# Performance work log

Measured on AMD Instinct MI355X. Metric: run time of the kernel, lower is better.

## Reference

```python
import jax, jax.numpy as jnp
import numpy as np

TH, TL = 0.85, 0.5          # sim thresholds
ALPHA = 0.1                 # proto EMA alpha
TEMP = 1.0                  # readout temperature
KEEP, REFINE, REPLACE, SPAWN = 0, 1, 2, 3


def _l2n(x, axis=-1):
    return x / jnp.maximum(jnp.linalg.norm(x, axis=axis, keepdims=True), 1e-12)


def setup_inputs() -> dict:
    key = jax.random.key(0)
    ks = jax.random.split(key, 12)
    B, N, C, H, W, K = 4, 8, 256, 64, 64, 16
    return {
        "value_BNCHW": jax.random.normal(ks[0], (B, N, C, H, W), jnp.float32),
        "frame_feat_BCHW": jax.random.normal(ks[1], (B, C, H, W), jnp.float32),
        "mask_BNHW": jax.random.uniform(ks[2], (B, N, H, W), jnp.float32),
        "proto": jax.random.normal(ks[3], (B, N, K, C), jnp.float32),
        "age": jax.random.uniform(ks[4], (B, N, K), jnp.float32) * 10.0,
        "usage": jax.random.uniform(ks[5], (B, N, K), jnp.float32) * 5.0,
        "conf": jax.random.uniform(ks[6], (B, N, K), jnp.float32),
        "valid": jax.random.bernoulli(ks[7], 0.7, (B, N, K)),
        "W1": jax.random.normal(ks[8], (C + K + 3 * K, 256), jnp.float32) * 0.02,
        "b1": jnp.zeros((256,), jnp.float32),
        "W2": jax.random.normal(ks[9], (256, 4), jnp.float32) * 0.02,
        "b2": jnp.zeros((4,), jnp.float32),
        "proto_gate": jnp.float32(1.0),
        "frame_gate": jnp.float32(1.0),
    }


def reference(value_BNCHW, frame_feat_BCHW, mask_BNHW, proto, age, usage, conf,
              valid, W1, b1, W2, b2, proto_gate, frame_gate):
    B, N, C, H, W = value_BNCHW.shape
    K = proto.shape[2]
    P = H * W

    # ---- candidate prototype: masked mean pool over HW ----
    flat_v = value_BNCHW.reshape(B, N, C, P)          # [B,N,C,P]
    flat_m = mask_BNHW.reshape(B, N, 1, P)            # [B,N,1,P]
    denom = flat_m.sum(-1)                            # [B,N,1]
    cand = (flat_v * flat_m).sum(-1) / jnp.maximum(denom, 1e-6)
    fallback = flat_v.mean(-1)
    cand = jnp.where(denom <= 1e-5, fallback, cand)   # [B,N,C]
    mask_strength = flat_m.mean(-1)[..., 0]           # [B,N]
    cand = _l2n(cand)

    # ---- cosine sim against bank + context ----
    norm_bank = _l2n(proto)
    sim = jnp.einsum('bnc,bnkc->bnk', cand, norm_bank)
    sim = jnp.where(valid, sim, -1.0)
    g_t = frame_feat_BCHW.mean((2, 3))                # [B,C]
    age_n = age / jnp.maximum(jax.lax.stop_gradient(age.max()), 1.0)
    use_n = usage / jnp.maximum(jax.lax.stop_gradient(usage.max()), 1.0)
    stats = jnp.stack([age_n, use_n, conf], -1).reshape(B, N, 3 * K)
    context = jnp.concatenate(
        [jnp.broadcast_to(g_t[:, None, :], (B, N, C)), sim, stats], -1)
    any_valid = valid.any(-1)
    target_slot = jnp.where(any_valid, sim.argmax(-1), 0)
    max_sim = jnp.take_along_axis(sim, target_slot[..., None], -1)[..., 0]
    max_sim = jnp.where(any_valid, max_sim, 0.0)

    # ---- policy MLP (logits logged; rule-based policy selects action) ----
    logits = jax.nn.gelu(context @ W1 + b1) @ W2 + b2  # [B,N,4]

    has_free = (~valid).any(-1)
    low = max_sim < TL
    action = jnp.full((B, N), REFINE, jnp.int32)
    action = jnp.where(max_sim > TH, KEEP, action)
    action = jnp.where(low & has_free, SPAWN, action)
    action = jnp.where(low & ~has_free, REPLACE, action)

    # ---- action-conditioned slot selection + scatter update ----
    worst = jnp.argmax(age - usage - conf + 1000.0 * (~valid), -1)
    free_slot = jnp.argmax(~valid, -1)
    spawn = action == SPAWN
    replace = action == REPLACE
    refine = action == REFINE
    keep = action == KEEP
    chosen = target_slot
    chosen = jnp.where(spawn & has_free, free_slot, chosen)
    chosen = jnp.where(spawn & ~has_free, worst, chosen)   # spawn_replace_when_full
    chosen = jnp.where(replace, worst, chosen)
    update = refine | replace | spawn
    replace_like = replace | spawn

    bi = jnp.arange(B)[:, None]
    ni = jnp.arange(N)[None, :]

    old_p = proto[bi, ni, chosen]                      # [B,N,C] gather
    refined = _l2n((1.0 - ALPHA) * old_p + ALPHA * cand)
    new_p = jnp.where(refine[..., None], refined,
                      jnp.where(replace_like[..., None], cand, old_p))
    proto_new = proto.at[bi, ni, chosen].set(new_p)

    age1 = age + 1.0
    age_new = age1.at[bi, ni, chosen].set(
        jnp.where(replace_like, 0.0, age1[bi, ni, chosen]))
    usage_new = usage.at[bi, ni, chosen].set(
        jnp.where(replace_like, 1.0,
                  usage[bi, ni, chosen] + (refine | keep).astype(jnp.float32)))
    conf_g = conf[bi, ni, chosen]
    conf_val = jnp.where(refine, jnp.clip(0.5 * conf_g + 0.5 * max_sim, 0.0, 1.0),
                         jnp.where(replace_like, jnp.clip(mask_strength, 0.0, 1.0),
                                   conf_g))
    conf_new = conf.at[bi, ni, chosen].set(conf_val)
    valid_new = valid.at[bi, ni, chosen].set(valid[bi, ni, chosen] | update)

    # ---- prototype-conditioned readout (softmax over bank slots per pixel) ----
    vn = flat_v / jnp.maximum(jnp.linalg.norm(flat_v, axis=2, keepdims=True), 1e-12)
    nb = _l2n(proto_new)
    scores = jnp.einsum('bnkc,bncp->bnkp', nb, vn) / TEMP
    scores = jnp.where(valid_new[..., None], scores, -1e9)
    wts = jax.nn.softmax(scores, axis=2)               # over K
    proto_map = jnp.einsum('bnkp,bnkc->bncp', wts, proto_new)
    proto_map = jnp.where(valid_new.any(-1)[:, :, None, None], proto_map, 0.0)
    proto_map = proto_map.reshape(B, N, C, H, W)

    conditioned = (value_BNCHW + proto_gate * proto_map
                   + frame_gate * frame_feat_BCHW[:, None])
    return conditioned, logits
```

## Files before the change

### kernel.cpp

```cpp
#include <hip/hip_runtime.h>
#include <math.h>

#define NB_B 4
#define NB_N 8
#define NB_C 256
#define NB_K 16
#define NB_P 4096
#define NB_BN (NB_B * NB_N)

typedef float nfloat4 __attribute__((ext_vector_type(4)));

#define WS_WSUM 0
#define WS_VSUM (NB_BN * NB_C)
#define WS_GT   (2 * NB_BN * NB_C)
#define WS_DEN  (WS_GT + NB_B * NB_C)
#define WS_NB   17440
#define WS_PN   (WS_NB + NB_BN * NB_K * NB_C)
#define WS_VAL  (WS_PN + NB_BN * NB_K * NB_C)

#define SLAB_STRIDE 516

__device__ __forceinline__ float2 blk_sum2(float a, float b, float2* sbuf) {
#pragma unroll
  for (int off = 32; off > 0; off >>= 1) {
    a += __shfl_down(a, off, 64);
    b += __shfl_down(b, off, 64);
  }
  int lane = threadIdx.x & 63, wid = threadIdx.x >> 6;
  __syncthreads();
  if (lane == 0) sbuf[wid] = make_float2(a, b);
  __syncthreads();
  float2 r;
  r.x = sbuf[0].x + sbuf[1].x + sbuf[2].x + sbuf[3].x;
  r.y = sbuf[0].y + sbuf[1].y + sbuf[2].y + sbuf[3].y;
  return r;
}

__device__ __forceinline__ float2 blk_max2(float a, float b, float2* sbuf) {
#pragma unroll
  for (int off = 32; off > 0; off >>= 1) {
    a = fmaxf(a, __shfl_down(a, off, 64));
    b = fmaxf(b, __shfl_down(b, off, 64));
  }
  int lane = threadIdx.x & 63, wid = threadIdx.x >> 6;
  __syncthreads();
  if (lane == 0) sbuf[wid] = make_float2(a, b);
  __syncthreads();
  float2 r;
  r.x = fmaxf(fmaxf(sbuf[0].x, sbuf[1].x), fmaxf(sbuf[2].x, sbuf[3].x));
  r.y = fmaxf(fmaxf(sbuf[0].y, sbuf[1].y), fmaxf(sbuf[2].y, sbuf[3].y));
  return r;
}

__device__ __forceinline__ int validMode(const void* vptr) {
  const unsigned int* w = (const unsigned int*)vptr;
  int mode = 0;
  for (int i = 0; i < 128; ++i) {
    unsigned int x = w[i];
    if (x == 0x3f800000u) return 2;
    if (x > 1u) mode = 1;
  }
  return mode;
}
__device__ __forceinline__ bool getValid(const void* vptr, int mode, int idx) {
  if (mode == 1) return ((const unsigned char*)vptr)[idx] != 0;
  if (mode == 2) return ((const float*)vptr)[idx] != 0.0f;
  return ((const int*)vptr)[idx] != 0;
}

__global__ __launch_bounds__(256) void k1_reduce(
    const float* __restrict__ value, const float* __restrict__ frame,
    const float* __restrict__ mask, float* __restrict__ ws) {
  __shared__ float2 sbuf[4];
  int gid = blockIdx.x, tid = threadIdx.x;
  if (gid < NB_BN * NB_C) {
    int bn = gid >> 8;
    const float4* v4 = (const float4*)(value + (size_t)gid * NB_P);
    const float4* m4 = (const float4*)(mask + (size_t)bn * NB_P);
    float wsum = 0.f, vsum = 0.f;
#pragma unroll
    for (int i = 0; i < NB_P / 4 / 256; ++i) {
      float4 a = v4[i * 256 + tid];
      float4 m = m4[i * 256 + tid];
      wsum += a.x * m.x + a.y * m.y + a.z * m.z + a.w * m.w;
      vsum += a.x + a.y + a.z + a.w;
    }
    float2 r = blk_sum2(wsum, vsum, sbuf);
    if (tid == 0) { ws[WS_WSUM + gid] = r.x; ws[WS_VSUM + gid] = r.y; }
  } else if (gid < NB_BN * NB_C + NB_B * NB_C) {
    int idx = gid - NB_BN * NB_C;
    const float4* f4 = (const float4*)(frame + (size_t)idx * NB_P);
    float s = 0.f;
#pragma unroll
    for (int i = 0; i < 4; ++i) {
      float4 a = f4[i * 256 + tid];
      s += a.x + a.y + a.z + a.w;
    }
    float2 r = blk_sum2(s, 0.f, sbuf);
    if (tid == 0) ws[WS_GT + idx] = r.x * (1.0f / NB_P);
  } else {
    int bn = gid - NB_BN * NB_C - NB_B * NB_C;
    const float4* m4 = (const float4*)(mask + (size_t)bn * NB_P);
    float s = 0.f;
#pragma unroll
    for (int i = 0; i < 4; ++i) {
      float4 a = m4[i * 256 + tid];
      s += a.x + a.y + a.z + a.w;
    }
    float2 r = blk_sum2(s, 0.f, sbuf);
    if (tid == 0) ws[WS_DEN + bn] = r.x;
  }
}

__global__ __launch_bounds__(256) void k2_policy(
    const float* __restrict__ proto, const float* __restrict__ age,
    const float* __restrict__ usage, const float* __restrict__ conf,
    const void* __restrict__ valid, const float* __restrict__ W1,
    const float* __restrict__ b1, const float* __restrict__ W2,
    const float* __restrict__ b2, float* __restrict__ ws,
    float* __restrict__ out_logits) {
  __shared__ float2 sbuf[4];
  __shared__ float s_cand[NB_C];
  __shared__ float s_sim[NB_K];
  __shared__ float s_invn[NB_K];
  __shared__ float s_ctx[NB_C + NB_K + 3 * NB_K];
  __shared__ int s_dec[4];
  __shared__ int s_vmode;

  int bn = blockIdx.x;
  int b = bn >> 3;
  int c = threadIdx.x;
  if (c == 0) s_vmode = validMode(valid);

  float denom = ws[WS_DEN + bn];
  float cand;
  if (denom <= 1e-5f) cand = ws[WS_VSUM + bn * NB_C + c] * (1.0f / NB_P);
  else                cand = ws[WS_WSUM + bn * NB_C + c] / fmaxf(denom, 1e-6f);
  float2 r0 = blk_sum2(cand * cand, 0.f, sbuf);
  cand *= 1.0f / fmaxf(sqrtf(r0.x), 1e-12f);
  s_cand[c] = cand;
  __syncthreads();
  int vmode = s_vmode;

  const float* pr = proto + (size_t)bn * NB_K * NB_C;
  {
    int wid = c >> 6, lane = c & 63;
#pragma unroll
    for (int q = 0; q < 4; ++q) {
      int k = wid * 4 + q;
      float pp = 0.f, pc = 0.f;
#pragma unroll
      for (int t = 0; t < 4; ++t) {
        int cc = lane + t * 64;
        float p = pr[k * NB_C + cc];
        pp += p * p;
        pc += p * s_cand[cc];
      }
#pragma unroll
      for (int off = 32; off > 0; off >>= 1) {
        pp += __shfl_down(pp, off, 64);
        pc += __shfl_down(pc, off, 64);
      }
      if (lane == 0) {
        float invk = 1.0f / fmaxf(sqrtf(pp), 1e-12f);
        s_invn[k] = invk;
        s_sim[k] = getValid(valid, vmode, bn * NB_K + k) ? pc * invk : -1.0f;
      }
    }
  }

  float am = fmaxf(age[c], age[c + 256]);
  float um = fmaxf(usage[c], usage[c + 256]);
  float2 mx = blk_max2(am, um, sbuf);
  float age_max = fmaxf(mx.x, 1.0f);
  float use_max = fmaxf(mx.y, 1.0f);

  s_ctx[c] = ws[WS_GT + b * NB_C + c];
  if (c < NB_K) {
    int k = c;
    s_ctx[NB_C + k] = s_sim[k];
    s_ctx[NB_C + NB_K + 3 * k + 0] = age[bn * NB_K + k] / age_max;
    s_ctx[NB_C + NB_K + 3 * k + 1] = usage[bn * NB_K + k] / use_max;
    s_ctx[NB_C + NB_K + 3 * k + 2] = conf[bn * NB_K + k];
  }
  __syncthreads();

  float acc = b1[c];
  for (int i = 0; i < NB_C + 4 * NB_K; ++i) acc += s_ctx[i] * W1[i * 256 + c];
  float h = 0.5f * acc *
            (1.0f + tanhf(0.7978845608028654f * (acc + 0.044715f * acc * acc * acc)));
  for (int j = 0; j < 4; ++j) {
    float2 lj = blk_sum2(h * W2[c * 4 + j], 0.f, sbuf);
    if (c == 0) out_logits[bn * 4 + j] = lj.x + b2[j];
  }

  if (c == 0) {
    bool anyv = false, hasfree = false;
    for (int k = 0; k < NB_K; ++k) {
      if (getValid(valid, vmode, bn * NB_K + k)) anyv = true; else hasfree = true;
    }
    int tgt = 0; float best = s_sim[0];
    for (int k = 1; k < NB_K; ++k) if (s_sim[k] > best) { best = s_sim[k]; tgt = k; }
    if (!anyv) tgt = 0;
    float max_sim = anyv ? s_sim[tgt] : 0.0f;
    int action = 1;
    if (max_sim > 0.85f) action = 0;
    bool low = max_sim < 0.5f;
    if (low && hasfree) action = 3;
    if (low && !hasfree) action = 2;
    int worst = 0; float wb = -1e30f;
    for (int k = 0; k < NB_K; ++k) {
      float sc = age[bn * NB_K + k] - usage[bn * NB_K + k] - conf[bn * NB_K + k] +
                 (getValid(valid, vmode, bn * NB_K + k) ? 0.f : 1000.f);
      if (sc > wb) { wb = sc; worst = k; }
    }
    int freeslot = 0;
    for (int k = 0; k < NB_K; ++k) {
      if (!getValid(valid, vmode, bn * NB_K + k)) { freeslot = k; break; }
    }
    int chosen = tgt;
    if (action == 3) chosen = hasfree ? freeslot : worst;
    if (action == 2) chosen = worst;
    s_dec[0] = chosen;
    s_dec[1] = (action == 1);
    s_dec[2] = (action == 2 || action == 3);
    s_dec[3] = (action != 0);
  }
  __syncthreads();

  int chosen = s_dec[0];
  float oldp = pr[chosen * NB_C + c];
  float t = 0.9f * oldp + 0.1f * s_cand[c];
  float2 tn = blk_sum2(t * t, 0.f, sbuf);
  float invt = 1.0f / fmaxf(sqrtf(tn.x), 1e-12f);
  float pn_chosen = s_dec[1] ? t * invt : (s_dec[2] ? s_cand[c] : oldp);
  float nb_chosen = s_dec[1] ? t * invt
                   : (s_dec[2] ? s_cand[c] : oldp * s_invn[chosen]);
  float nbrow[NB_K], pnrow[NB_K];
#pragma unroll
  for (int k = 0; k < NB_K; ++k) {
    float praw = pr[k * NB_C + c];
    nbrow[k] = (k == chosen) ? nb_chosen : praw * s_invn[k];
    pnrow[k] = (k == chosen) ? pn_chosen : praw;
  }
  float* nbp = ws + WS_NB + (size_t)bn * NB_K * NB_C + c * NB_K;
  float* pnp = ws + WS_PN + (size_t)bn * NB_K * NB_C + c * NB_K;
#pragma unroll
  for (int q = 0; q < 4; ++q) {
    *(float4*)(nbp + 4 * q) =
        make_float4(nbrow[4 * q], nbrow[4 * q + 1], nbrow[4 * q + 2], nbrow[4 * q + 3]);
    *(float4*)(pnp + 4 * q) =
        make_float4(pnrow[4 * q], pnrow[4 * q + 1], pnrow[4 * q + 2], pnrow[4 * q + 3]);
  }
  if (c < NB_K) {
    bool v = getValid(valid, vmode, bn * NB_K + c) || (c == chosen && s_dec[3]);
    ws[WS_VAL + bn * NB_K + c] = v ? 1.0f : 0.0f;
  }
}

__global__ __launch_bounds__(256) void k3_fused(
    const float* __restrict__ value, const float* __restrict__ frame,
    const float* __restrict__ ws, const float* __restrict__ pgp,
    const float* __restrict__ fgp, float* __restrict__ out) {
  __shared__ float s_bank[8 * SLAB_STRIDE];
  int blk = blockIdx.x;
  int bn = blk >> 5, pxchunk = blk & 31;
  int b = bn >> 3;
  int tid = threadIdx.x;
  int lane = tid & 63, wv = tid >> 6;
  int slab = lane >> 3, pxg = lane & 7;
  int px = pxchunk * 128 + wv * 32 + pxg * 4;
  int cbase = slab * 32;

  const float4* nb4 = (const float4*)(ws + WS_NB + (size_t)bn * NB_K * NB_C);
  const float4* pn4 = (const float4*)(ws + WS_PN + (size_t)bn * NB_K * NB_C);
#pragma unroll
  for (int j = 0; j < 4; ++j) {
    int f = j * 256 + tid;
    int c = f >> 2, k4 = f & 3;
    *(float4*)(s_bank + (c >> 5) * SLAB_STRIDE + (c & 31) * 16 + k4 * 4) = nb4[f];
  }
  int vmask = 0;
  for (int k = 0; k < NB_K; ++k)
    if (ws[WS_VAL + bn * NB_K + k] != 0.0f) vmask |= (1 << k);
  float pg = pgp[0], fg = fgp[0];
  __syncthreads();

  const float* vp = value + ((size_t)bn * NB_C + cbase) * NB_P + px;
  const float* snb = s_bank + slab * SLAB_STRIDE;
  float4 d[NB_K];
#pragma unroll
  for (int k = 0; k < NB_K; ++k) d[k] = make_float4(0.f, 0.f, 0.f, 0.f);
  float4 ss = make_float4(0.f, 0.f, 0.f, 0.f);
#pragma unroll 4
  for (int c = 0; c < 32; ++c) {
    float4 v = *(const float4*)(vp + (size_t)c * NB_P);
    ss.x += v.x * v.x; ss.y += v.y * v.y; ss.z += v.z * v.z; ss.w += v.w * v.w;
    const float4* nrow = (const float4*)(snb + c * 16);
    float4 n0 = nrow[0], n1 = nrow[1], n2 = nrow[2], n3 = nrow[3];
#define ACC(K, S)                                                        \
    d[K].x += v.x * S; d[K].y += v.y * S; d[K].z += v.z * S; d[K].w += v.w * S;
    ACC(0, n0.x)  ACC(1, n0.y)  ACC(2, n0.z)  ACC(3, n0.w)
    ACC(4, n1.x)  ACC(5, n1.y)  ACC(6, n1.z)  ACC(7, n1.w)
    ACC(8, n2.x)  ACC(9, n2.y)  ACC(10, n2.z) ACC(11, n2.w)
    ACC(12, n3.x) ACC(13, n3.y) ACC(14, n3.z) ACC(15, n3.w)
#undef ACC
  }
  __syncthreads();

#pragma unroll
  for (int j = 0; j < 4; ++j) {
    int f = j * 256 + tid;
    int c = f >> 2, k4 = f & 3;
    *(float4*)(s_bank + (c >> 5) * SLAB_STRIDE + (c & 31) * 16 + k4 * 4) = pn4[f];
  }

#pragma unroll
  for (int mask = 8; mask <= 32; mask <<= 1) {
#pragma unroll
    for (int k = 0; k < NB_K; ++k) {
      d[k].x += __shfl_xor(d[k].x, mask, 64);
      d[k].y += __shfl_xor(d[k].y, mask, 64);
      d[k].z += __shfl_xor(d[k].z, mask, 64);
      d[k].w += __shfl_xor(d[k].w, mask, 64);
    }
    ss.x += __shfl_xor(ss.x, mask, 64);
    ss.y += __shfl_xor(ss.y, mask, 64);
    ss.z += __shfl_xor(ss.z, mask, 64);
    ss.w += __shfl_xor(ss.w, mask, 64);
  }

  float4 invv;
  invv.x = 1.0f / fmaxf(sqrtf(ss.x), 1e-12f);
  invv.y = 1.0f / fmaxf(sqrtf(ss.y), 1e-12f);
  invv.z = 1.0f / fmaxf(sqrtf(ss.z), 1e-12f);
  invv.w = 1.0f / fmaxf(sqrtf(ss.w), 1e-12f);
  float4 m = make_float4(-1e30f, -1e30f, -1e30f, -1e30f);
#pragma unroll
  for (int k = 0; k < NB_K; ++k) {
    d[k].x *= invv.x; d[k].y *= invv.y; d[k].z *= invv.z; d[k].w *= invv.w;
    if ((vmask >> k) & 1) {
      m.x = fmaxf(m.x, d[k].x); m.y = fmaxf(m.y, d[k].y);
      m.z = fmaxf(m.z, d[k].z); m.w = fmaxf(m.w, d[k].w);
    }
  }
  float4 es = make_float4(0.f, 0.f, 0.f, 0.f);
#pragma unroll
  for (int k = 0; k < NB_K; ++k) {
    if ((vmask >> k) & 1) {
      d[k].x = __expf(d[k].x - m.x); d[k].y = __expf(d[k].y - m.y);
      d[k].z = __expf(d[k].z - m.z); d[k].w = __expf(d[k].w - m.w);
      es.x += d[k].x; es.y += d[k].y; es.z += d[k].z; es.w += d[k].w;
    } else {
      d[k] = make_float4(0.f, 0.f, 0.f, 0.f);
    }
  }
  float4 isum;
  isum.x = vmask ? (1.0f / es.x) : 0.0f;
  isum.y = vmask ? (1.0f / es.y) : 0.0f;
  isum.z = vmask ? (1.0f / es.z) : 0.0f;
  isum.w = vmask ? (1.0f / es.w) : 0.0f;
#pragma unroll
  for (int k = 0; k < NB_K; ++k) {
    d[k].x *= isum.x; d[k].y *= isum.y; d[k].z *= isum.z; d[k].w *= isum.w;
  }
  __syncthreads();

  const float* fp = frame + ((size_t)b * NB_C + cbase) * NB_P + px;
  float* op = out + ((size_t)bn * NB_C + cbase) * NB_P + px;
  const float* spn = s_bank + slab * SLAB_STRIDE;
#pragma unroll 2
  for (int c = 0; c < 32; ++c) {
    float4 v = *(const float4*)(vp + (size_t)c * NB_P);
    float4 f = *(const float4*)(fp + (size_t)c * NB_P);
    const float4* prow = (const float4*)(spn + c * 16);
    float4 p0 = prow[0], p1 = prow[1], p2 = prow[2], p3 = prow[3];
    float4 pm = make_float4(0.f, 0.f, 0.f, 0.f);
#define APM(K, S)                                                        \
    pm.x += d[K].x * S; pm.y += d[K].y * S; pm.z += d[K].z * S; pm.w += d[K].w * S;
    APM(0, p0.x)  APM(1, p0.y)  APM(2, p0.z)  APM(3, p0.w)
    APM(4, p1.x)  APM(5, p1.y)  APM(6, p1.z)  APM(7, p1.w)
    APM(8, p2.x)  APM(9, p2.y)  APM(10, p2.z) APM(11, p2.w)
    APM(12, p3.x) APM(13, p3.y) APM(14, p3.z) APM(15, p3.w)
#undef APM
    nfloat4 o;
    o.x = v.x + pg * pm.x + fg * f.x;
    o.y = v.y + pg * pm.y + fg * f.y;
    o.z = v.z + pg * pm.z + fg * f.z;
    o.w = v.w + pg * pm.w + fg * f.w;
    __builtin_nontemporal_store(o, (nfloat4*)(op + (size_t)c * NB_P));
  }
}

extern "C" void kernel_launch(void* const* d_in, const int* in_sizes, int n_in,
                              void* d_out, int out_size, void* d_ws, size_t ws_size,
                              hipStream_t stream) {
  const float* value = (const float*)d_in[0];
  const float* frame = (const float*)d_in[1];
  const float* mask  = (const float*)d_in[2];
  const float* proto = (const float*)d_in[3];
  const float* age   = (const float*)d_in[4];
  const float* usage = (const float*)d_in[5];
  const float* conf  = (const float*)d_in[6];
  const void*  valid = (const void*)d_in[7];
  const float* W1 = (const float*)d_in[8];
  const float* b1 = (const float*)d_in[9];
  const float* W2 = (const float*)d_in[10];
  const float* b2 = (const float*)d_in[11];
  const float* pg = (const float*)d_in[12];
  const float* fg = (const float*)d_in[13];
  float* out = (float*)d_out;
  float* ws = (float*)d_ws;

  int g1 = NB_BN * NB_C + NB_B * NB_C + NB_BN;
  hipLaunchKernelGGL(k1_reduce, dim3(g1), dim3(256), 0, stream,
                     value, frame, mask, ws);
  hipLaunchKernelGGL(k2_policy, dim3(NB_BN), dim3(256), 0, stream,
                     proto, age, usage, conf, valid, W1, b1, W2, b2, ws,
                     out + (size_t)NB_BN * NB_C * NB_P);
  hipLaunchKernelGGL(k3_fused, dim3(NB_BN * 32), dim3(256), 0, stream,
                     value, frame, ws, pg, fg, out);
}
```

Before: 137.9 us.

## Stream value and frame tiles through per-wave LDS ring via async global-to-LDS loads

Replaces the direct global float4 loads in both passes of k3_fused with a per-wave LDS ring buffer, filled ahead of use by global_load_lds instructions and guarded by explicit vmcnt waits. The score pass keeps seven rows in flight and the output pass keeps three value/frame row pairs in flight. The aim is to hide HBM latency behind the FMA work without spending registers on prefetch. In exchange it adds 32KB of LDS per block, which can lower occupancy, and it relies on exact vmcnt counting and on LDS writes being visible without a barrier.

Result: slower. 143.0 us (+3.7%).

```diff
diff --git a/kernel.cpp b/kernel.cpp
--- a/kernel.cpp
+++ b/kernel.cpp
@@ -19,6 +19,12 @@
 #define WS_VAL  (WS_PN + NB_BN * NB_K * NB_C)
 
 #define SLAB_STRIDE 516
+
+__device__ __forceinline__ void stage16(const float* g, float* l) {
+  __builtin_amdgcn_global_load_lds(
+      (const __attribute__((address_space(1))) unsigned int*)g,
+      (__attribute__((address_space(3))) unsigned int*)l, 16, 0, 0);
+}
 
 __device__ __forceinline__ float2 blk_sum2(float a, float b, float2* sbuf) {
 #pragma unroll
@@ -258,11 +264,15 @@
   }
 }
 
+#define VMWAIT(n) asm volatile("s_waitcnt vmcnt(" #n ")" ::: "memory"); \
+                  __builtin_amdgcn_sched_barrier(0)
+
 __global__ __launch_bounds__(256) void k3_fused(
     const float* __restrict__ value, const float* __restrict__ frame,
     const float* __restrict__ ws, const float* __restrict__ pgp,
     const float* __restrict__ fgp, float* __restrict__ out) {
   __shared__ float s_bank[8 * SLAB_STRIDE];
+  __shared__ float s_ring[4][8][256];
   int blk = blockIdx.x;
   int bn = blk >> 5, pxchunk = blk & 31;
   int b = bn >> 3;
@@ -271,6 +281,7 @@
   int slab = lane >> 3, pxg = lane & 7;
   int px = pxchunk * 128 + wv * 32 + pxg * 4;
   int cbase = slab * 32;
+  float* myring = &s_ring[wv][0][0];
 
   const float4* nb4 = (const float4*)(ws + WS_NB + (size_t)bn * NB_K * NB_C);
   const float4* pn4 = (const float4*)(ws + WS_PN + (size_t)bn * NB_K * NB_C);
@@ -284,28 +295,52 @@
   for (int k = 0; k < NB_K; ++k)
     if (ws[WS_VAL + bn * NB_K + k] != 0.0f) vmask |= (1 << k);
   float pg = pgp[0], fg = fgp[0];
-  __syncthreads();
 
   const float* vp = value + ((size_t)bn * NB_C + cbase) * NB_P + px;
+  const float* fp = frame + ((size_t)b * NB_C + cbase) * NB_P + px;
+  float* op = out + ((size_t)bn * NB_C + cbase) * NB_P + px;
   const float* snb = s_bank + slab * SLAB_STRIDE;
+
+#pragma unroll
+  for (int r = 0; r < 7; ++r)
+    stage16(vp + (size_t)r * NB_P, myring + r * 256);
+  __syncthreads();
+
   float4 d[NB_K];
 #pragma unroll
   for (int k = 0; k < NB_K; ++k) d[k] = make_float4(0.f, 0.f, 0.f, 0.f);
   float4 ss = make_float4(0.f, 0.f, 0.f, 0.f);
-#pragma unroll 4
-  for (int c = 0; c < 32; ++c) {
-    float4 v = *(const float4*)(vp + (size_t)c * NB_P);
-    ss.x += v.x * v.x; ss.y += v.y * v.y; ss.z += v.z * v.z; ss.w += v.w * v.w;
-    const float4* nrow = (const float4*)(snb + c * 16);
-    float4 n0 = nrow[0], n1 = nrow[1], n2 = nrow[2], n3 = nrow[3];
-#define ACC(K, S)                                                        \
+
+#define BODY1(c)                                                          \
+  {                                                                       \
+    float4 v = *(const float4*)(myring + ((c) & 7) * 256 + (lane << 2));  \
+    if ((c) < 25) stage16(vp + (size_t)((c) + 7) * NB_P,                  \
+                          myring + (((c) + 7) & 7) * 256);                \
+    ss.x += v.x * v.x; ss.y += v.y * v.y;                                 \
+    ss.z += v.z * v.z; ss.w += v.w * v.w;                                 \
+    const float4* nrow = (const float4*)(snb + (c) * 16);                 \
+    float4 n0 = nrow[0], n1 = nrow[1], n2 = nrow[2], n3 = nrow[3];        \
+    ACC(0, n0.x)  ACC(1, n0.y)  ACC(2, n0.z)  ACC(3, n0.w)                \
+    ACC(4, n1.x)  ACC(5, n1.y)  ACC(6, n1.z)  ACC(7, n1.w)                \
+    ACC(8, n2.x)  ACC(9, n2.y)  ACC(10, n2.z) ACC(11, n2.w)               \
+    ACC(12, n3.x) ACC(13, n3.y) ACC(14, n3.z) ACC(15, n3.w)               \
+  }
+#define ACC(K, S)                                                         \
     d[K].x += v.x * S; d[K].y += v.y * S; d[K].z += v.z * S; d[K].w += v.w * S;
-    ACC(0, n0.x)  ACC(1, n0.y)  ACC(2, n0.z)  ACC(3, n0.w)
-    ACC(4, n1.x)  ACC(5, n1.y)  ACC(6, n1.z)  ACC(7, n1.w)
-    ACC(8, n2.x)  ACC(9, n2.y)  ACC(10, n2.z) ACC(11, n2.w)
-    ACC(12, n3.x) ACC(13, n3.y) ACC(14, n3.z) ACC(15, n3.w)
+
+  for (int c = 0; c < 26; ++c) {
+    VMWAIT(6);
+    BODY1(c);
+  }
+  { VMWAIT(5); BODY1(26); }
+  { VMWAIT(4); BODY1(27); }
+  { VMWAIT(3); BODY1(28); }
+  { VMWAIT(2); BODY1(29); }
+  { VMWAIT(1); BODY1(30); }
+  { VMWAIT(0); BODY1(31); }
 #undef ACC
-  }
+#undef BODY1
+
   __syncthreads();
 
 #pragma unroll
@@ -313,6 +348,11 @@
     int f = j * 256 + tid;
     int c = f >> 2, k4 = f & 3;
     *(float4*)(s_bank + (c >> 5) * SLAB_STRIDE + (c & 31) * 16 + k4 * 4) = pn4[f];
+  }
+#pragma unroll
+  for (int r = 0; r < 3; ++r) {
+    stage16(vp + (size_t)r * NB_P, myring + (r * 2) * 256);
+    stage16(fp + (size_t)r * NB_P, myring + (r * 2 + 1) * 256);
   }
 
 #pragma unroll
@@ -366,30 +406,40 @@
   }
   __syncthreads();
 
-  const float* fp = frame + ((size_t)b * NB_C + cbase) * NB_P + px;
-  float* op = out + ((size_t)bn * NB_C + cbase) * NB_P + px;
-  const float* spn = s_bank + slab * SLAB_STRIDE;
-#pragma unroll 2
-  for (int c = 0; c < 32; ++c) {
-    float4 v = *(const float4*)(vp + (size_t)c * NB_P);
-    float4 f = *(const float4*)(fp + (size_t)c * NB_P);
-    const float4* prow = (const float4*)(spn + c * 16);
-    float4 p0 = prow[0], p1 = prow[1], p2 = prow[2], p3 = prow[3];
-    float4 pm = make_float4(0.f, 0.f, 0.f, 0.f);
-#define APM(K, S)                                                        \
+#define BODY2(c)                                                          \
+  {                                                                       \
+    float4 v = *(const float4*)(myring + (((c) & 3) * 2) * 256 + (lane << 2));   \
+    float4 f = *(const float4*)(myring + (((c) & 3) * 2 + 1) * 256 + (lane << 2)); \
+    if ((c) < 29) {                                                       \
+      int r_ = (c) + 3;                                                   \
+      stage16(vp + (size_t)r_ * NB_P, myring + ((r_ & 3) * 2) * 256);     \
+      stage16(fp + (size_t)r_ * NB_P, myring + ((r_ & 3) * 2 + 1) * 256); \
+    }                                                                     \
+    const float4* prow = (const float4*)(snb + (c) * 16);                 \
+    float4 p0 = prow[0], p1 = prow[1], p2 = prow[2], p3 = prow[3];        \
+    float4 pm = make_float4(0.f, 0.f, 0.f, 0.f);                          \
+    APM(0, p0.x)  APM(1, p0.y)  APM(2, p0.z)  APM(3, p0.w)                \
+    APM(4, p1.x)  APM(5, p1.y)  APM(6, p1.z)  APM(7, p1.w)                \
+    APM(8, p2.x)  APM(9, p2.y)  APM(10, p2.z) APM(11, p2.w)               \
+    APM(12, p3.x) APM(13, p3.y) APM(14, p3.z) APM(15, p3.w)               \
+    nfloat4 o;                                                            \
+    o.x = v.x + pg * pm.x + fg * f.x;                                     \
+    o.y = v.y + pg * pm.y + fg * f.y;                                     \
+    o.z = v.z + pg * pm.z + fg * f.z;                                     \
+    o.w = v.w + pg * pm.w + fg * f.w;                                     \
+    __builtin_nontemporal_store(o, (nfloat4*)(op + (size_t)(c) * NB_P));  \
+  }
+#define APM(K, S)                                                         \
     pm.x += d[K].x * S; pm.y += d[K].y * S; pm.z += d[K].z * S; pm.w += d[K].w * S;
-    APM(0, p0.x)  APM(1, p0.y)  APM(2, p0.z)  APM(3, p0.w)
-    APM(4, p1.x)  APM(5, p1.y)  APM(6, p1.z)  APM(7, p1.w)
-    APM(8, p2.x)  APM(9, p2.y)  APM(10, p2.z) APM(11, p2.w)
-    APM(12, p3.x) APM(13, p3.y) APM(14, p3.z) APM(15, p3.w)
+
+  for (int c = 0; c < 30; ++c) {
+    VMWAIT(7);
+    BODY2(c);
+  }
+  { VMWAIT(5); BODY2(30); }
+  { VMWAIT(3); BODY2(31); }
 #undef APM
-    nfloat4 o;
-    o.x = v.x + pg * pm.x + fg * f.x;
-    o.y = v.y + pg * pm.y + fg * f.y;
-    o.z = v.z + pg * pm.z + fg * f.z;
-    o.w = v.w + pg * pm.w + fg * f.w;
-    __builtin_nontemporal_store(o, (nfloat4*)(op + (size_t)c * NB_P));
-  }
+#undef BODY2
 }
 
 extern "C" void kernel_launch(void* const* d_in, const int* in_sizes, int n_in,
```
